# Optimization experiments

Hardware: AMD Instinct MI355X
Metric: run time of the kernel (lower is better)

Reference implementation:

```python
import jax, jax.numpy as jnp
import numpy as np

N, E, D = 50000, 300000, 256
BN_EPS = 1e-5


def setup_inputs() -> dict:
    key = jax.random.key(0)
    ks = jax.random.split(key, 8)
    s = 1.0 / np.sqrt(D)
    return {
        'x': jax.random.normal(ks[0], (N, D), dtype=jnp.float32),
        'edge_index': jax.random.randint(ks[1], (2, E), 0, N, dtype=jnp.int64),
        'edge_attr': jax.random.normal(ks[2], (E, D), dtype=jnp.float32),
        'W1': jax.random.normal(ks[3], (D, D), dtype=jnp.float32) * s,
        'b1': jnp.zeros((D,), jnp.float32),
        'W2': jax.random.normal(ks[4], (D, D), dtype=jnp.float32) * s,
        'b2': jnp.zeros((D,), jnp.float32),
        'bn1_gamma': jnp.ones((D,), jnp.float32),
        'bn1_beta': jnp.zeros((D,), jnp.float32),
        'bn1_mean': jnp.zeros((D,), jnp.float32),
        'bn1_var': jnp.ones((D,), jnp.float32),
        'bn2_gamma': jnp.ones((D,), jnp.float32),
        'bn2_beta': jnp.zeros((D,), jnp.float32),
        'bn2_mean': jnp.zeros((D,), jnp.float32),
        'bn2_var': jnp.ones((D,), jnp.float32),
    }


def _bn(z, gamma, beta, mean, var):
    # eval-mode BatchNorm1d
    return (z - mean) * jax.lax.rsqrt(var + BN_EPS) * gamma + beta


def reference(x, edge_index, edge_attr, W1, b1, W2, b2,
              bn1_gamma, bn1_beta, bn1_mean, bn1_var,
              bn2_gamma, bn2_beta, bn2_mean, bn2_var):
    src, dst = edge_index[0], edge_index[1]
    # GINEConv message: relu(x_j + edge_attr), scatter-sum at destination
    msg = jax.nn.relu(x[src] + edge_attr)                      # [E, D]
    agg = jax.ops.segment_sum(msg, dst, num_segments=x.shape[0])  # [N, D]
    conv_out = x + agg            # (1+eps)*x + agg, eps=0; nn=Dropout is identity in eval
    h = x + conv_out              # residual: data.x + conv output
    # FFN: BN -> Linear -> GELU -> Linear
    f = _bn(h, bn1_gamma, bn1_beta, bn1_mean, bn1_var)
    f = jax.nn.gelu(f @ W1.T + b1, approximate=False)
    f = f @ W2.T + b2
    return _bn(h + f, bn2_gamma, bn2_beta, bn2_mean, bn2_var)
```

## Files before the change

### kernel.cpp

```cpp
#include <hip/hip_runtime.h>
#include <hip/hip_bf16.h>
#include <math.h>

#define D 256
#define D4 64
#define GS 264

typedef __attribute__((ext_vector_type(8))) short bf16x8;
typedef __attribute__((ext_vector_type(4))) float f32x4;

__device__ inline unsigned short f2bf(float f) {
    union { float f; unsigned u; } v; v.f = f;
    unsigned r = v.u + 0x7fffu + ((v.u >> 16) & 1u);
    return (unsigned short)(r >> 16);
}
__device__ inline float bf2f(unsigned short u) {
    union { unsigned u; float f; } v; v.u = ((unsigned)u) << 16; return v.f;
}
__device__ inline float gelu_tanh(float t) {
    float z = 0.7978845608028654f * (t + 0.044715f * t * t * t);
    float e = __expf(2.f * z);
    return 0.5f * t * (2.f - 2.f / (e + 1.f));
}
__device__ inline f32x4 ntload4(const float4* p) {
    return __builtin_nontemporal_load((const f32x4*)p);
}

__global__ __launch_bounds__(256) void k_prep(
    const float* __restrict__ W1, const float* __restrict__ W2,
    unsigned short* __restrict__ W1b, unsigned short* __restrict__ W2b,
    const float* g1, const float* be1, const float* m1, const float* v1,
    const float* g2, const float* be2, const float* m2, const float* v2,
    float* s1, float* sh1, float* r1, float* s2, float* sh2,
    int* counts, int N_)
{
    int i = blockIdx.x * 256 + threadIdx.x;
    if (i < D * D) {
        W1b[i] = f2bf(W1[i]);
        W2b[i] = f2bf(W2[i]);
    }
    if (i < N_) counts[i] = 0;
    if (i < D) {
        float sc1 = g1[i] * rsqrtf(v1[i] + 1e-5f);
        s1[i] = sc1; sh1[i] = be1[i] - m1[i] * sc1; r1[i] = 1.f / sc1;
        float sc2 = g2[i] * rsqrtf(v2[i] + 1e-5f);
        s2[i] = sc2; sh2[i] = be2[i] - m2[i] * sc2;
    }
}

__global__ __launch_bounds__(256) void k_hist(const int* __restrict__ ei, int* counts, int E_) {
    int e = blockIdx.x * 256 + threadIdx.x;
    if (e < E_) atomicAdd(&counts[ei[E_ + e]], 1);
}

__global__ __launch_bounds__(256) void k_scan1(const int* __restrict__ counts,
                                               int* offs, int* partials, int n) {
    __shared__ int tmp[256];
    int tid = threadIdx.x, i = blockIdx.x * 256 + tid;
    int v = (i < n) ? counts[i] : 0;
    tmp[tid] = v; __syncthreads();
    for (int d = 1; d < 256; d <<= 1) {
        int t = (tid >= d) ? tmp[tid - d] : 0;
        __syncthreads();
        tmp[tid] += t;
        __syncthreads();
    }
    if (i < n) offs[i] = tmp[tid] - v;
    if (tid == 255) partials[blockIdx.x] = tmp[255];
}

__global__ __launch_bounds__(256) void k_scan23(int* offs, int* cursor,
                                                const int* __restrict__ partials,
                                                int nb, int n, int E_) {
    __shared__ int red[256];
    int tid = threadIdx.x;
    int v = 0;
    for (int t = tid; t < nb; t += 256)
        if (t < (int)blockIdx.x) v += partials[t];
    red[tid] = v; __syncthreads();
    for (int d = 128; d > 0; d >>= 1) {
        if (tid < d) red[tid] += red[tid + d];
        __syncthreads();
    }
    int prefix = red[0];
    int i = blockIdx.x * 256 + tid;
    if (i < n) {
        int val = offs[i] + prefix;
        offs[i] = val;
        cursor[i] = val;
    }
    if (i == 0) offs[n] = E_;
}

__global__ __launch_bounds__(256) void k_bucket(const int* __restrict__ ei,
                                                int* cursor, int2* sorted, int E_) {
    int e = blockIdx.x * 256 + threadIdx.x;
    if (e < E_) {
        int d = ei[E_ + e];
        int pos = atomicAdd(&cursor[d], 1);
        sorted[pos] = make_int2(ei[e], e);
    }
}

__global__ __launch_bounds__(256) void k_fused(
    const float4* __restrict__ x, const float4* __restrict__ ea,
    const int* __restrict__ offs, const int2* __restrict__ sorted,
    const float* __restrict__ s1, const float* __restrict__ sh1,
    const float* __restrict__ r1,
    const unsigned short* __restrict__ W1, const unsigned short* __restrict__ W2,
    const float* __restrict__ b1, const float* __restrict__ b2,
    const float* __restrict__ s2, const float* __restrict__ sh2,
    float* __restrict__ out, int M)
{
    __shared__ __align__(16) unsigned short As[16][GS];
    __shared__ __align__(16) unsigned short Gsm[16][GS];

    int wave = threadIdx.x >> 6, lane = threadIdx.x & 63;
    int m_base = blockIdx.x * 16;

    float4 sc1v = ((const float4*)s1)[lane];
    float4 sh1v = ((const float4*)sh1)[lane];
#pragma unroll
    for (int rr = 0; rr < 4; ++rr) {
        int tr = wave * 4 + rr;
        int row = m_base + tr;
        if (row < M) {
            float4 xv = x[(long)row * D4 + lane];
            float ax = 2.f * xv.x, ay = 2.f * xv.y, az = 2.f * xv.z, aw = 2.f * xv.w;
            int b = offs[row], en = offs[row + 1];
            int done = b;
            while (done < en) {
                int rem = en - done;
                int chunk = rem < 64 ? rem : 64;
                int lidx = lane < chunk ? lane : chunk - 1;
                int2 se = sorted[done + lidx];
                int j = 0;
                for (; j + 4 <= chunk; j += 4) {
                    int p0 = __shfl(se.x, j    ), q0 = __shfl(se.y, j    );
                    int p1 = __shfl(se.x, j + 1), q1 = __shfl(se.y, j + 1);
                    int p2 = __shfl(se.x, j + 2), q2 = __shfl(se.y, j + 2);
                    int p3 = __shfl(se.x, j + 3), q3 = __shfl(se.y, j + 3);
                    float4 s0 = x[(long)p0 * D4 + lane];
                    f32x4  a0 = ntload4(&ea[(long)q0 * D4 + lane]);
                    float4 s1v = x[(long)p1 * D4 + lane];
                    f32x4  a1 = ntload4(&ea[(long)q1 * D4 + lane]);
                    float4 s2v = x[(long)p2 * D4 + lane];
                    f32x4  a2 = ntload4(&ea[(long)q2 * D4 + lane]);
                    float4 s3v = x[(long)p3 * D4 + lane];
                    f32x4  a3 = ntload4(&ea[(long)q3 * D4 + lane]);
                    ax += fmaxf(s0.x + a0.x, 0.f) + fmaxf(s1v.x + a1.x, 0.f)
                        + fmaxf(s2v.x + a2.x, 0.f) + fmaxf(s3v.x + a3.x, 0.f);
                    ay += fmaxf(s0.y + a0.y, 0.f) + fmaxf(s1v.y + a1.y, 0.f)
                        + fmaxf(s2v.y + a2.y, 0.f) + fmaxf(s3v.y + a3.y, 0.f);
                    az += fmaxf(s0.z + a0.z, 0.f) + fmaxf(s1v.z + a1.z, 0.f)
                        + fmaxf(s2v.z + a2.z, 0.f) + fmaxf(s3v.z + a3.z, 0.f);
                    aw += fmaxf(s0.w + a0.w, 0.f) + fmaxf(s1v.w + a1.w, 0.f)
                        + fmaxf(s2v.w + a2.w, 0.f) + fmaxf(s3v.w + a3.w, 0.f);
                }
                for (; j + 2 <= chunk; j += 2) {
                    int p0 = __shfl(se.x, j    ), q0 = __shfl(se.y, j    );
                    int p1 = __shfl(se.x, j + 1), q1 = __shfl(se.y, j + 1);
                    float4 s0 = x[(long)p0 * D4 + lane];
                    f32x4  a0 = ntload4(&ea[(long)q0 * D4 + lane]);
                    float4 s1v = x[(long)p1 * D4 + lane];
                    f32x4  a1 = ntload4(&ea[(long)q1 * D4 + lane]);
                    ax += fmaxf(s0.x + a0.x, 0.f) + fmaxf(s1v.x + a1.x, 0.f);
                    ay += fmaxf(s0.y + a0.y, 0.f) + fmaxf(s1v.y + a1.y, 0.f);
                    az += fmaxf(s0.z + a0.z, 0.f) + fmaxf(s1v.z + a1.z, 0.f);
                    aw += fmaxf(s0.w + a0.w, 0.f) + fmaxf(s1v.w + a1.w, 0.f);
                }
                if (j < chunk) {
                    int p0 = __shfl(se.x, j), q0 = __shfl(se.y, j);
                    float4 s0 = x[(long)p0 * D4 + lane];
                    f32x4  a0 = ntload4(&ea[(long)q0 * D4 + lane]);
                    ax += fmaxf(s0.x + a0.x, 0.f);
                    ay += fmaxf(s0.y + a0.y, 0.f);
                    az += fmaxf(s0.z + a0.z, 0.f);
                    aw += fmaxf(s0.w + a0.w, 0.f);
                }
                done += chunk;
            }
            ushort4 o;
            o.x = f2bf(ax * sc1v.x + sh1v.x);
            o.y = f2bf(ay * sc1v.y + sh1v.y);
            o.z = f2bf(az * sc1v.z + sh1v.z);
            o.w = f2bf(aw * sc1v.w + sh1v.w);
            *(ushort4*)&As[tr][lane * 4] = o;
        }
    }
    __syncthreads();

    int l16 = lane & 15, quad = lane >> 4;

    bf16x8 frag[8];
#pragma unroll
    for (int s = 0; s < 8; ++s)
        frag[s] = *(const bf16x8*)&As[l16][quad * 8 + s * 32];

#pragma unroll
    for (int t = 0; t < 4; ++t) {
        int ncol = (wave * 4 + t) * 16 + l16;
        const bf16x8* Wrow = (const bf16x8*)(W1 + ((long)ncol * D + quad * 8));
        f32x4 acc0 = {0.f, 0.f, 0.f, 0.f};
        f32x4 acc1 = {0.f, 0.f, 0.f, 0.f};
#pragma unroll
        for (int s = 0; s < 8; s += 2) {
            acc0 = __builtin_amdgcn_mfma_f32_16x16x32_bf16(frag[s],     Wrow[s * 4],       acc0, 0, 0, 0);
            acc1 = __builtin_amdgcn_mfma_f32_16x16x32_bf16(frag[s + 1], Wrow[(s + 1) * 4], acc1, 0, 0, 0);
        }
        float b = b1[ncol];
#pragma unroll
        for (int r = 0; r < 4; ++r) {
            float v = acc0[r] + acc1[r] + b;
            Gsm[quad * 4 + r][ncol] = f2bf(gelu_tanh(v));
        }
    }
    __syncthreads();

#pragma unroll
    for (int s = 0; s < 8; ++s)
        frag[s] = *(const bf16x8*)&Gsm[l16][quad * 8 + s * 32];

#pragma unroll
    for (int t = 0; t < 4; ++t) {
        int ncol = (wave * 4 + t) * 16 + l16;
        const bf16x8* Wrow = (const bf16x8*)(W2 + ((long)ncol * D + quad * 8));
        f32x4 acc0 = {0.f, 0.f, 0.f, 0.f};
        f32x4 acc1 = {0.f, 0.f, 0.f, 0.f};
#pragma unroll
        for (int s = 0; s < 8; s += 2) {
            acc0 = __builtin_amdgcn_mfma_f32_16x16x32_bf16(frag[s],     Wrow[s * 4],       acc0, 0, 0, 0);
            acc1 = __builtin_amdgcn_mfma_f32_16x16x32_bf16(frag[s + 1], Wrow[(s + 1) * 4], acc1, 0, 0, 0);
        }
        float b = b2[ncol], rr1 = r1[ncol], sh = sh1[ncol];
        float c2 = s2[ncol], h2 = sh2[ncol];
#pragma unroll
        for (int r = 0; r < 4; ++r) {
            int tr = quad * 4 + r;
            int row = m_base + tr;
            if (row < M) {
                float f = acc0[r] + acc1[r] + b;
                float hv = (bf2f(As[tr][ncol]) - sh) * rr1;
                __builtin_nontemporal_store((hv + f) * c2 + h2, &out[(long)row * D + ncol]);
            }
        }
    }
}

extern "C" void kernel_launch(void* const* d_in, const int* in_sizes, int n_in,
                              void* d_out, int out_size, void* d_ws, size_t ws_size,
                              hipStream_t stream) {
    const float* x   = (const float*)d_in[0];
    const int*   ei  = (const int*)d_in[1];
    const float* ea  = (const float*)d_in[2];
    const float* W1  = (const float*)d_in[3];
    const float* b1  = (const float*)d_in[4];
    const float* W2  = (const float*)d_in[5];
    const float* b2  = (const float*)d_in[6];
    const float* g1  = (const float*)d_in[7];
    const float* be1 = (const float*)d_in[8];
    const float* m1  = (const float*)d_in[9];
    const float* v1  = (const float*)d_in[10];
    const float* g2  = (const float*)d_in[11];
    const float* be2 = (const float*)d_in[12];
    const float* m2  = (const float*)d_in[13];
    const float* v2  = (const float*)d_in[14];
    float* out = (float*)d_out;

    int N_ = in_sizes[0] / D;
    int E_ = in_sizes[2] / D;

    char* ws = (char*)d_ws;
    size_t off = 0;
    unsigned short* W1b = (unsigned short*)(ws + off);  off += (size_t)D * D * 2;
    unsigned short* W2b = (unsigned short*)(ws + off);  off += (size_t)D * D * 2;
    float* s1  = (float*)(ws + off); off += D * 4;
    float* sh1 = (float*)(ws + off); off += D * 4;
    float* r1  = (float*)(ws + off); off += D * 4;
    float* s2  = (float*)(ws + off); off += D * 4;
    float* sh2 = (float*)(ws + off); off += D * 4;
    int* counts   = (int*)(ws + off); off += (size_t)N_ * 4;
    int* cursor   = (int*)(ws + off); off += (size_t)N_ * 4;
    int* offs     = (int*)(ws + off); off += (size_t)(N_ + 1) * 4;
    int* partials = (int*)(ws + off); off += 256 * 4;
    int2* sorted  = (int2*)(ws + off); off += (size_t)E_ * 8;

    int nblkN = (N_ + 255) / 256;
    int nblkE = (E_ + 255) / 256;

    k_prep<<<(D * D + 255) / 256, 256, 0, stream>>>(W1, W2, W1b, W2b,
        g1, be1, m1, v1, g2, be2, m2, v2, s1, sh1, r1, s2, sh2, counts, N_);
    k_hist<<<nblkE, 256, 0, stream>>>(ei, counts, E_);
    k_scan1<<<nblkN, 256, 0, stream>>>(counts, offs, partials, N_);
    k_scan23<<<nblkN, 256, 0, stream>>>(offs, cursor, partials, nblkN, N_, E_);
    k_bucket<<<nblkE, 256, 0, stream>>>(ei, cursor, sorted, E_);

    int mtiles = (N_ + 15) / 16;
    k_fused<<<mtiles, 256, 0, stream>>>((const float4*)x, (const float4*)ea,
        offs, sorted, s1, sh1, r1, W1b, W2b, b1, b2, s2, sh2, out, N_);
}
```

Baseline: 602.6 us.

## Interleave gather across four rows per wave and reuse shared buffer

The edge gather now processes the four rows owned by a wave together. Each iteration issues loads for one edge of every row, with masking for rows that have fewer edges, so more independent memory requests are in flight. Rows with more than 64 edges fall back to a per-row loop. The second shared-memory buffer is dropped by caching the residual h values in registers and reusing As for the GELU output, which lowers LDS usage to allow higher occupancy at the cost of more registers and an extra barrier.

Result: slower. 630.4 us (+4.6%).

```diff
diff --git a/kernel.cpp b/kernel.cpp
--- a/kernel.cpp
+++ b/kernel.cpp
@@ -113,80 +113,107 @@
     float* __restrict__ out, int M)
 {
     __shared__ __align__(16) unsigned short As[16][GS];
-    __shared__ __align__(16) unsigned short Gsm[16][GS];
 
     int wave = threadIdx.x >> 6, lane = threadIdx.x & 63;
     int m_base = blockIdx.x * 16;
+    int row0 = m_base + wave * 4;
 
     float4 sc1v = ((const float4*)s1)[lane];
     float4 sh1v = ((const float4*)sh1)[lane];
-#pragma unroll
-    for (int rr = 0; rr < 4; ++rr) {
-        int tr = wave * 4 + rr;
-        int row = m_base + tr;
+
+    int bb[5];
+#pragma unroll
+    for (int r = 0; r < 5; ++r) {
+        int rr = row0 + r; if (rr > M) rr = M;
+        bb[r] = offs[rr];
+    }
+
+    f32x4 acc[4];
+    int dd[4];
+    int2 se[4];
+    bool fast = true;
+#pragma unroll
+    for (int r = 0; r < 4; ++r) {
+        dd[r] = bb[r + 1] - bb[r];
+        if (dd[r] > 64) fast = false;
+        int row = row0 + r;
         if (row < M) {
             float4 xv = x[(long)row * D4 + lane];
-            float ax = 2.f * xv.x, ay = 2.f * xv.y, az = 2.f * xv.z, aw = 2.f * xv.w;
-            int b = offs[row], en = offs[row + 1];
-            int done = b;
+            acc[r].x = 2.f * xv.x; acc[r].y = 2.f * xv.y;
+            acc[r].z = 2.f * xv.z; acc[r].w = 2.f * xv.w;
+        } else {
+            acc[r].x = 0.f; acc[r].y = 0.f; acc[r].z = 0.f; acc[r].w = 0.f;
+        }
+        int li = lane < dd[r] ? lane : dd[r] - 1;
+        int idx = (dd[r] > 0) ? (bb[r] + li) : 0;
+        se[r] = sorted[idx];
+    }
+
+    if (fast) {
+        int dmax = dd[0] > dd[1] ? dd[0] : dd[1];
+        if (dd[2] > dmax) dmax = dd[2];
+        if (dd[3] > dmax) dmax = dd[3];
+        for (int k = 0; k < dmax; ++k) {
+            int p[4], q[4]; float m[4];
+#pragma unroll
+            for (int r = 0; r < 4; ++r) {
+                int kk = k < dd[r] ? k : (dd[r] > 0 ? dd[r] - 1 : 0);
+                p[r] = __shfl(se[r].x, kk);
+                q[r] = __shfl(se[r].y, kk);
+                m[r] = (k < dd[r]) ? 1.f : 0.f;
+            }
+            float4 sv0 = x[(long)p[0] * D4 + lane]; f32x4 av0 = ntload4(&ea[(long)q[0] * D4 + lane]);
+            float4 sv1 = x[(long)p[1] * D4 + lane]; f32x4 av1 = ntload4(&ea[(long)q[1] * D4 + lane]);
+            float4 sv2 = x[(long)p[2] * D4 + lane]; f32x4 av2 = ntload4(&ea[(long)q[2] * D4 + lane]);
+            float4 sv3 = x[(long)p[3] * D4 + lane]; f32x4 av3 = ntload4(&ea[(long)q[3] * D4 + lane]);
+            acc[0].x += m[0] * fmaxf(sv0.x + av0.x, 0.f);
+            acc[0].y += m[0] * fmaxf(sv0.y + av0.y, 0.f);
+            acc[0].z += m[0] * fmaxf(sv0.z + av0.z, 0.f);
+            acc[0].w += m[0] * fmaxf(sv0.w + av0.w, 0.f);
+            acc[1].x += m[1] * fmaxf(sv1.x + av1.x, 0.f);
+            acc[1].y += m[1] * fmaxf(sv1.y + av1.y, 0.f);
+            acc[1].z += m[1] * fmaxf(sv1.z + av1.z, 0.f);
+            acc[1].w += m[1] * fmaxf(sv1.w + av1.w, 0.f);
+            acc[2].x += m[2] * fmaxf(sv2.x + av2.x, 0.f);
+            acc[2].y += m[2] * fmaxf(sv2.y + av2.y, 0.f);
+            acc[2].z += m[2] * fmaxf(sv2.z + av2.z, 0.f);
+            acc[2].w += m[2] * fmaxf(sv2.w + av2.w, 0.f);
+            acc[3].x += m[3] * fmaxf(sv3.x + av3.x, 0.f);
+            acc[3].y += m[3] * fmaxf(sv3.y + av3.y, 0.f);
+            acc[3].z += m[3] * fmaxf(sv3.z + av3.z, 0.f);
+            acc[3].w += m[3] * fmaxf(sv3.w + av3.w, 0.f);
+        }
+    } else {
+#pragma unroll
+        for (int r = 0; r < 4; ++r) {
+            int done = bb[r], en = bb[r + 1];
             while (done < en) {
                 int rem = en - done;
                 int chunk = rem < 64 ? rem : 64;
-                int lidx = lane < chunk ? lane : chunk - 1;
-                int2 se = sorted[done + lidx];
-                int j = 0;
-                for (; j + 4 <= chunk; j += 4) {
-                    int p0 = __shfl(se.x, j    ), q0 = __shfl(se.y, j    );
-                    int p1 = __shfl(se.x, j + 1), q1 = __shfl(se.y, j + 1);
-                    int p2 = __shfl(se.x, j + 2), q2 = __shfl(se.y, j + 2);
-                    int p3 = __shfl(se.x, j + 3), q3 = __shfl(se.y, j + 3);
-                    float4 s0 = x[(long)p0 * D4 + lane];
-                    f32x4  a0 = ntload4(&ea[(long)q0 * D4 + lane]);
-                    float4 s1v = x[(long)p1 * D4 + lane];
-                    f32x4  a1 = ntload4(&ea[(long)q1 * D4 + lane]);
-                    float4 s2v = x[(long)p2 * D4 + lane];
-                    f32x4  a2 = ntload4(&ea[(long)q2 * D4 + lane]);
-                    float4 s3v = x[(long)p3 * D4 + lane];
-                    f32x4  a3 = ntload4(&ea[(long)q3 * D4 + lane]);
-                    ax += fmaxf(s0.x + a0.x, 0.f) + fmaxf(s1v.x + a1.x, 0.f)
-                        + fmaxf(s2v.x + a2.x, 0.f) + fmaxf(s3v.x + a3.x, 0.f);
-                    ay += fmaxf(s0.y + a0.y, 0.f) + fmaxf(s1v.y + a1.y, 0.f)
-                        + fmaxf(s2v.y + a2.y, 0.f) + fmaxf(s3v.y + a3.y, 0.f);
-                    az += fmaxf(s0.z + a0.z, 0.f) + fmaxf(s1v.z + a1.z, 0.f)
-                        + fmaxf(s2v.z + a2.z, 0.f) + fmaxf(s3v.z + a3.z, 0.f);
-                    aw += fmaxf(s0.w + a0.w, 0.f) + fmaxf(s1v.w + a1.w, 0.f)
-                        + fmaxf(s2v.w + a2.w, 0.f) + fmaxf(s3v.w + a3.w, 0.f);
-                }
-                for (; j + 2 <= chunk; j += 2) {
-                    int p0 = __shfl(se.x, j    ), q0 = __shfl(se.y, j    );
-                    int p1 = __shfl(se.x, j + 1), q1 = __shfl(se.y, j + 1);
-                    float4 s0 = x[(long)p0 * D4 + lane];
-                    f32x4  a0 = ntload4(&ea[(long)q0 * D4 + lane]);
-                    float4 s1v = x[(long)p1 * D4 + lane];
-                    f32x4  a1 = ntload4(&ea[(long)q1 * D4 + lane]);
-                    ax += fmaxf(s0.x + a0.x, 0.f) + fmaxf(s1v.x + a1.x, 0.f);
-                    ay += fmaxf(s0.y + a0.y, 0.f) + fmaxf(s1v.y + a1.y, 0.f);
-                    az += fmaxf(s0.z + a0.z, 0.f) + fmaxf(s1v.z + a1.z, 0.f);
-                    aw += fmaxf(s0.w + a0.w, 0.f) + fmaxf(s1v.w + a1.w, 0.f);
-                }
-                if (j < chunk) {
-                    int p0 = __shfl(se.x, j), q0 = __shfl(se.y, j);
-                    float4 s0 = x[(long)p0 * D4 + lane];
-                    f32x4  a0 = ntload4(&ea[(long)q0 * D4 + lane]);
-                    ax += fmaxf(s0.x + a0.x, 0.f);
-                    ay += fmaxf(s0.y + a0.y, 0.f);
-                    az += fmaxf(s0.z + a0.z, 0.f);
-                    aw += fmaxf(s0.w + a0.w, 0.f);
+                int li2 = lane < chunk ? lane : chunk - 1;
+                int2 sc = sorted[done + li2];
+                for (int j = 0; j < chunk; ++j) {
+                    int pp = __shfl(sc.x, j), qq = __shfl(sc.y, j);
+                    float4 sv = x[(long)pp * D4 + lane];
+                    f32x4  av = ntload4(&ea[(long)qq * D4 + lane]);
+                    acc[r].x += fmaxf(sv.x + av.x, 0.f);
+                    acc[r].y += fmaxf(sv.y + av.y, 0.f);
+                    acc[r].z += fmaxf(sv.z + av.z, 0.f);
+                    acc[r].w += fmaxf(sv.w + av.w, 0.f);
                 }
                 done += chunk;
             }
-            ushort4 o;
-            o.x = f2bf(ax * sc1v.x + sh1v.x);
-            o.y = f2bf(ay * sc1v.y + sh1v.y);
-            o.z = f2bf(az * sc1v.z + sh1v.z);
-            o.w = f2bf(aw * sc1v.w + sh1v.w);
-            *(ushort4*)&As[tr][lane * 4] = o;
-        }
+        }
+    }
+
+#pragma unroll
+    for (int r = 0; r < 4; ++r) {
+        ushort4 o;
+        o.x = f2bf(acc[r].x * sc1v.x + sh1v.x);
+        o.y = f2bf(acc[r].y * sc1v.y + sh1v.y);
+        o.z = f2bf(acc[r].z * sc1v.z + sh1v.z);
+        o.w = f2bf(acc[r].w * sc1v.w + sh1v.w);
+        *(ushort4*)&As[wave * 4 + r][lane * 4] = o;
     }
     __syncthreads();
 
@@ -196,6 +223,16 @@
 #pragma unroll
     for (int s = 0; s < 8; ++s)
         frag[s] = *(const bf16x8*)&As[l16][quad * 8 + s * 32];
+
+    float h_res[4][4];
+#pragma unroll
+    for (int t = 0; t < 4; ++t) {
+        int ncol = (wave * 4 + t) * 16 + l16;
+#pragma unroll
+        for (int r = 0; r < 4; ++r)
+            h_res[t][r] = bf2f(As[quad * 4 + r][ncol]);
+    }
+    __syncthreads();
 
 #pragma unroll
     for (int t = 0; t < 4; ++t) {
@@ -212,14 +249,14 @@
 #pragma unroll
         for (int r = 0; r < 4; ++r) {
             float v = acc0[r] + acc1[r] + b;
-            Gsm[quad * 4 + r][ncol] = f2bf(gelu_tanh(v));
+            As[quad * 4 + r][ncol] = f2bf(gelu_tanh(v));
         }
     }
     __syncthreads();
 
 #pragma unroll
     for (int s = 0; s < 8; ++s)
-        frag[s] = *(const bf16x8*)&Gsm[l16][quad * 8 + s * 32];
+        frag[s] = *(const bf16x8*)&As[l16][quad * 8 + s * 32];
 
 #pragma unroll
     for (int t = 0; t < 4; ++t) {
@@ -236,11 +273,10 @@
         float c2 = s2[ncol], h2 = sh2[ncol];
 #pragma unroll
         for (int r = 0; r < 4; ++r) {
-            int tr = quad * 4 + r;
-            int row = m_base + tr;
+            int row = m_base + quad * 4 + r;
             if (row < M) {
                 float f = acc0[r] + acc1[r] + b;
-                float hv = (bf2f(As[tr][ncol]) - sh) * rr1;
+                float hv = (h_res[t][r] - sh) * rr1;
                 __builtin_nontemporal_store((hv + f) * c2 + h2, &out[(long)row * D + ncol]);
             }
         }
```
